# Optimization experiments

Measured on AMD Instinct MI355X. Metric: run time of the kernel, lower is better.

Reference implementation:

```python
import jax, jax.numpy as jnp
import numpy as np

NUM_EXPERTS = 16
TOP_K = 2
FFT_LEN = 512
SEQ_LEN = 512
PRED_LEN = 720
MOE_TEMP = 1.0


def setup_inputs() -> dict:
    key = jax.random.key(0)
    ks = jax.random.split(key, 5)
    x = jax.random.normal(ks[0], (8192, SEQ_LEN), dtype=jnp.float32)
    # gating network: Linear(fft_len//2 -> num_experts)
    gw = jax.random.normal(ks[1], (NUM_EXPERTS, FFT_LEN // 2), dtype=jnp.float32) * (1.0 / np.sqrt(FFT_LEN // 2))
    gb = jnp.zeros((NUM_EXPERTS,), dtype=jnp.float32)
    # experts: RLinear = instance-norm (RevIN) + Linear(seq->pred), stacked
    ew = jax.random.normal(ks[2], (NUM_EXPERTS, SEQ_LEN, PRED_LEN), dtype=jnp.float32) * (1.0 / np.sqrt(SEQ_LEN))
    eb = jnp.zeros((NUM_EXPERTS, PRED_LEN), dtype=jnp.float32)
    return {"x": x, "gw": gw, "gb": gb, "ew": ew, "eb": eb}


def periodogram(x, n):
    # x: [B, L] -> normalized power spectrum [B, n//2]
    x0 = x - jnp.mean(x, axis=1, keepdims=True)
    dft = jnp.fft.fft(x0, n=n, axis=1) / jnp.sqrt(jnp.asarray(n, x.dtype))
    I = jnp.abs(dft[:, : n // 2]) ** 2
    s = jnp.sum(I, axis=1, keepdims=True)
    s = jnp.where(s == 0, 1.0, s)
    return I / s


def expert_apply(x, ew, eb):
    # RLinear: instance normalize, linear map, de-normalize
    mu = jnp.mean(x, axis=1, keepdims=True)
    sd = jnp.std(x, axis=1, keepdims=True) + 1e-5
    xn = (x - mu) / sd  # [B, L]
    # all experts densely: [B,L] x [E,L,P] -> [E,B,P]
    y = jnp.einsum('bl,elp->ebp', xn, ew) + eb[:, None, :]
    return y * sd[None] + mu[None]  # [E, B, P]


def reference(x, gw, gb, ew, eb):
    I = periodogram(x, FFT_LEN)  # [B, n//2]
    gate = (I @ gw.T + gb) / MOE_TEMP  # eval mode: divide by temp, no noise
    topk_vals, topk_idx = jax.lax.top_k(gate, TOP_K)  # [B, k]
    gates = jax.nn.softmax(topk_vals, axis=1)  # [B, k]
    expert_out = expert_apply(x, ew, eb)  # [E, B, P]
    # gather selected experts: [B, k, P]
    sel = jnp.take_along_axis(
        jnp.transpose(expert_out, (1, 0, 2)), topk_idx[:, :, None], axis=1
    )
    return jnp.sum(gates[:, :, None] * sel, axis=1)  # [B, P]
```

## Files before the change

### kernel.cpp

```cpp
#include <hip/hip_runtime.h>
#include <hip/hip_bf16.h>
#include <math.h>

#define NEXP  16
#define SEQ   512
#define PRED  720
#define NROWS 8192
#define NFREQ 256

typedef __bf16 bf16x8 __attribute__((ext_vector_type(8)));
typedef float  f32x16 __attribute__((ext_vector_type(16)));

__device__ __forceinline__ void gload_lds16(const void* g, void* l) {
    __builtin_amdgcn_global_load_lds(
        (const __attribute__((address_space(1))) unsigned int*)g,
        (__attribute__((address_space(3))) unsigned int*)l, 16, 0, 0);
}

__device__ __forceinline__ int xcd_swizzle(int bid, int nwg) {
    const int q = nwg >> 3, r = nwg & 7;
    const int xcd = bid & 7, off = bid >> 3;
    return (xcd < r ? xcd * (q + 1) : r * (q + 1) + (xcd - r) * q) + off;
}

__global__ __launch_bounds__(256) void k_preproc(const float* __restrict__ ew,
                                                 const float* __restrict__ x,
                                                 __hip_bfloat16* __restrict__ ewt,
                                                 __hip_bfloat16* __restrict__ bthi,
                                                 __hip_bfloat16* __restrict__ btlo,
                                                 __hip_bfloat16* __restrict__ xn,
                                                 __hip_bfloat16* __restrict__ xnlo,
                                                 float* __restrict__ meta,
                                                 int* __restrict__ nredo)
{
    const int bid = blockIdx.x;
    const int t   = threadIdx.x;

    if (bid < 512) {
        if (bid == 0 && t == 0) *nredo = 0;
        const int tid  = bid * 256 + t;
        const int f    = tid >> 9;
        const int lidx = tid & 511;
        const int m    = (f * lidx) & 511;

        constexpr double Cj[9] = {0.9999247018391445033, 0.9996988186962042201,
                                  0.9987954562051723927, 0.9951847266721968862,
                                  0.9807852804032304491, 0.9238795325112867561,
                                  0.7071067811865475244, 0.0, -1.0};
        constexpr double Sj[9] = {0.0122715382857199261, 0.0245412285229122880,
                                  0.0490676743274180143, 0.0980171403295606020,
                                  0.1950903220161282678, 0.3826834323650897717,
                                  0.7071067811865475244, 1.0, 0.0};
        double cr = 1.0, ci = 0.0;
#pragma unroll
        for (int j = 0; j < 9; ++j) {
            const bool on = (m >> j) & 1;
            const double mr = on ? Cj[j] : 1.0;
            const double mi = on ? Sj[j] : 0.0;
            const double nr = cr * mr - ci * mi;
            ci = cr * mi + ci * mr;
            cr = nr;
        }
        const size_t c0 = (size_t)(2 * f) * 512 + lidx;
        const size_t c1 = (size_t)(2 * f + 1) * 512 + lidx;
        {
            __hip_bfloat16 h = __float2bfloat16((float)cr);
            float hif = __bfloat162float(h);
            bthi[c0] = h;
            btlo[c0] = __float2bfloat16((float)(cr - (double)hif));
        }
        {
            __hip_bfloat16 h = __float2bfloat16((float)ci);
            float hif = __bfloat162float(h);
            bthi[c1] = h;
            btlo[c1] = __float2bfloat16((float)(ci - (double)hif));
        }
        return;
    }

    if (bid < 6400) {
        __shared__ float tile[32][33];
        const int rel = bid - 512;
        const int e   = rel / 368;
        const int rem = rel % 368;
        const int p0  = (rem % 23) * 32;
        const int l0  = (rem / 23) * 32;
        const int tx  = t & 31;
        const int ty  = t >> 5;
        const float* src = ew + (size_t)e * SEQ * PRED;
#pragma unroll
        for (int i = 0; i < 4; ++i) {
            int l = l0 + ty + i * 8;
            int p = p0 + tx;
            tile[ty + i * 8][tx] = (p < PRED) ? src[(size_t)l * PRED + p] : 0.f;
        }
        __syncthreads();
        __hip_bfloat16* dst = ewt + (size_t)e * PRED * SEQ;
#pragma unroll
        for (int i = 0; i < 4; ++i) {
            int p = p0 + ty + i * 8;
            int l = l0 + tx;
            if (p < PRED) dst[(size_t)p * SEQ + l] = __float2bfloat16(tile[tx][ty + i * 8]);
        }
        return;
    }

    {
        const int wv = t >> 6, l = t & 63;
        const int b  = (bid - 6400) * 4 + wv;
        const float* xr = x + (size_t)b * SEQ;

        const float4 v0 = *(const float4*)(xr + l * 8);
        const float4 v1 = *(const float4*)(xr + l * 8 + 4);
        const double d0 = v0.x, d1 = v0.y, d2 = v0.z, d3 = v0.w;
        const double d4 = v1.x, d5 = v1.y, d6 = v1.z, d7 = v1.w;

        double s1 = ((d0 + d1) + (d2 + d3)) + ((d4 + d5) + (d6 + d7));
        double s2 = ((d0 * d0 + d1 * d1) + (d2 * d2 + d3 * d3)) +
                    ((d4 * d4 + d5 * d5) + (d6 * d6 + d7 * d7));
#pragma unroll
        for (int off = 1; off < 64; off <<= 1) {
            s1 += __shfl_xor(s1, off);
            s2 += __shfl_xor(s2, off);
        }
        const double mu = s1 * (1.0 / 512.0);
        double var = s2 * (1.0 / 512.0) - mu * mu;
        if (var < 0.0) var = 0.0;
        const double sd = sqrt(var) + 1e-5, inv = 1.0 / sd;

        unsigned int hw[4], lw[4];
#define CONV(j, dj)                                                         \
        {                                                                   \
            double xnd = (dj - mu) * inv;                                   \
            __hip_bfloat16 h = __float2bfloat16((float)xnd);                \
            float hif = __bfloat162float(h);                                \
            __hip_bfloat16 lo = __float2bfloat16((float)(xnd - (double)hif)); \
            unsigned int hb = *(unsigned short*)&h;                         \
            unsigned int lb = *(unsigned short*)&lo;                        \
            if ((j & 1) == 0) { hw[j >> 1] = hb; lw[j >> 1] = lb; }         \
            else { hw[j >> 1] |= hb << 16; lw[j >> 1] |= lb << 16; }        \
        }
        CONV(0, d0) CONV(1, d1) CONV(2, d2) CONV(3, d3)
        CONV(4, d4) CONV(5, d5) CONV(6, d6) CONV(7, d7)
#undef CONV
        *(uint4*)(xn   + (size_t)b * SEQ + l * 8) = uint4{hw[0], hw[1], hw[2], hw[3]};
        *(uint4*)(xnlo + (size_t)b * SEQ + l * 8) = uint4{lw[0], lw[1], lw[2], lw[3]};

        if (l == 0) {
            meta[b * 4 + 0] = (float)mu;
            meta[b * 4 + 3] = (float)sd;
        }
    }
}

__global__ __launch_bounds__(256, 3) void k_dft_gemm(
    const __hip_bfloat16* __restrict__ xn, const __hip_bfloat16* __restrict__ xnlo,
    const __hip_bfloat16* __restrict__ bthi, const __hip_bfloat16* __restrict__ btlo,
    float* __restrict__ Iout)
{
    const int wgid = xcd_swizzle(blockIdx.x, 512);
    const int rt = wgid >> 2;
    const int ct = wgid & 3;

    __shared__ __align__(16) __hip_bfloat16 As[2][64][64];
    __shared__ __align__(16) __hip_bfloat16 Bs[2][128][64];

    const int t  = threadIdx.x;
    const int wv = t >> 6, l = t & 63;

    size_t aoff[2], boff[4];
    int arow[2], achk[2], brow[4], bchk[4];
#pragma unroll
    for (int i = 0; i < 2; ++i) {
        const int idx = i * 256 + t;
        const int row = idx >> 3, chk = idx & 7;
        const int swz = (row & 7) ^ ((row & 8) >> 1);
        arow[i] = row; achk[i] = chk;
        aoff[i] = (size_t)(rt * 64 + row) * SEQ + (size_t)(chk ^ swz) * 8;
    }
#pragma unroll
    for (int i = 0; i < 4; ++i) {
        const int idx = i * 256 + t;
        const int row = idx >> 3, chk = idx & 7;
        const int swz = (row & 7) ^ ((row & 8) >> 1);
        brow[i] = row; bchk[i] = chk;
        boff[i] = (size_t)(ct * 128 + row) * SEQ + (size_t)(chk ^ swz) * 8;
    }

#define DSTAGE(buf, kk) do {                                                   \
    const int pass_ = (kk) >> 3;                                               \
    const int koff_ = ((kk) & 7) * 64;                                         \
    const __hip_bfloat16* ap_ = (pass_ == 1) ? xnlo : xn;                      \
    const __hip_bfloat16* bp_ = (pass_ == 2) ? btlo : bthi;                    \
    _Pragma("unroll")                                                          \
    for (int i_ = 0; i_ < 2; ++i_)                                             \
        gload_lds16(ap_ + aoff[i_] + koff_, &As[buf][arow[i_]][achk[i_] * 8]); \
    _Pragma("unroll")                                                          \
    for (int i_ = 0; i_ < 4; ++i_)                                             \
        gload_lds16(bp_ + boff[i_] + koff_, &Bs[buf][brow[i_]][bchk[i_] * 8]); \
} while (0)

    f32x16 acc[2];
#pragma unroll
    for (int ni = 0; ni < 2; ++ni)
#pragma unroll
        for (int q = 0; q < 16; ++q) acc[ni][q] = 0.f;

    const int wr = wv >> 1, wc = wv & 1;
    const int fl = l & 31, fh = l >> 5;
    const int rswz = (fl & 7) ^ ((fl & 8) >> 1);

    DSTAGE(0, 0);
    asm volatile("s_waitcnt vmcnt(0)" ::: "memory");
    __builtin_amdgcn_s_barrier();
#pragma unroll
    for (int kt = 0; kt < 24; ++kt) {
        const int cur = kt & 1;
        if (kt < 23) DSTAGE(cur ^ 1, kt + 1);
        __builtin_amdgcn_sched_barrier(0);
        __builtin_amdgcn_s_setprio(1);
#pragma unroll
        for (int ks = 0; ks < 4; ++ks) {
            const int cc = ((ks * 2 + fh) ^ rswz) * 8;
            const bf16x8 a  = *(const bf16x8*)&As[cur][wr * 32 + fl][cc];
            const bf16x8 b0 = *(const bf16x8*)&Bs[cur][wc * 64 + fl][cc];
            const bf16x8 b1 = *(const bf16x8*)&Bs[cur][wc * 64 + 32 + fl][cc];
            acc[0] = __builtin_amdgcn_mfma_f32_32x32x16_bf16(a, b0, acc[0], 0, 0, 0);
            acc[1] = __builtin_amdgcn_mfma_f32_32x32x16_bf16(a, b1, acc[1], 0, 0, 0);
        }
        __builtin_amdgcn_s_setprio(0);
        __builtin_amdgcn_sched_barrier(0);
        asm volatile("s_waitcnt vmcnt(0)" ::: "memory");
        __builtin_amdgcn_s_barrier();
    }
#undef DSTAGE

    const int crow_base = 4 * fh;
#pragma unroll
    for (int ni = 0; ni < 2; ++ni) {
        const int col = ct * 128 + wc * 64 + ni * 32 + fl;
#pragma unroll
        for (int q = 0; q < 16; ++q) {
            const float v = acc[ni][q];
            const float w = __shfl_xor(v, 1);
            if ((fl & 1) == 0) {
                const int rl = wr * 32 + (q & 3) + 8 * (q >> 2) + crow_base;
                Iout[(size_t)(rt * 64 + rl) * NFREQ + (col >> 1)] = v * v + w * w;
            }
        }
    }
}

__global__ __launch_bounds__(256) void k_gatefin(const float* __restrict__ Iout,
                                                 const float* __restrict__ gw,
                                                 const float* __restrict__ gb,
                                                 float* __restrict__ meta,
                                                 int* __restrict__ eidx,
                                                 int* __restrict__ redo,
                                                 int* __restrict__ nredo)
{
    __shared__ float gws[NEXP * 257];
    __shared__ float Pw[4][256];
    __shared__ float Gs[4][16];

    const int t  = threadIdx.x;
    const int wv = t >> 6, l = t & 63;
    const int b  = blockIdx.x * 4 + wv;

    for (int i = t; i < NEXP * NFREQ; i += 256)
        gws[(i >> 8) * 257 + (i & 255)] = gw[i];
    __syncthreads();

    const float* Ir = Iout + (size_t)b * NFREQ;
    const float i0 = Ir[l], i1 = Ir[64 + l], i2 = Ir[128 + l], i3 = Ir[192 + l];
    Pw[wv][l] = i0; Pw[wv][64 + l] = i1; Pw[wv][128 + l] = i2; Pw[wv][192 + l] = i3;
    float ps = (i0 + i1) + (i2 + i3);
#pragma unroll
    for (int off = 1; off < 64; off <<= 1) ps += __shfl_xor(ps, off);

    const int e = l >> 2, kb = l & 3;
    float acc = 0.f;
#pragma unroll 8
    for (int j = 0; j < 64; ++j) {
        const int k = kb + 4 * j;
        acc += Pw[wv][k] * gws[e * 257 + k];
    }
    acc += __shfl_xor(acc, 1);
    acc += __shfl_xor(acc, 2);
    if (kb == 0) Gs[wv][e] = acc;

    if (l == 0) {
        const float sdiv  = (ps == 0.f) ? 1.f : ps;
        const float inv_s = 1.f / sdiv;
        float b1 = -1e30f, b2 = -1e30f, b3 = -1e30f;
        int i1b = 0, i2b = 0;
#pragma unroll
        for (int i = 0; i < NEXP; ++i) {
            float v = Gs[wv][i] * inv_s + gb[i];
            if (v > b1)      { b3 = b2; b2 = b1; i2b = i1b; b1 = v; i1b = i; }
            else if (v > b2) { b3 = b2; b2 = v; i2b = i; }
            else if (v > b3) { b3 = v; }
        }
        if (b2 - b3 < 1e-4f * fmaxf(1.f, fabsf(b1))) {
            const int r = atomicAdd(nredo, 1);
            redo[r] = b;
        } else {
            const float sd = meta[b * 4 + 3];
            const float ee = __expf(b2 - b1);
            const float w0 = 1.f / (1.f + ee);
            const float w1 = ee / (1.f + ee);
            meta[b * 4 + 1] = w0 * sd;
            meta[b * 4 + 2] = w1 * sd;
            eidx[b * 2 + 0] = i1b;
            eidx[b * 2 + 1] = i2b;
        }
    }
}

__global__ __launch_bounds__(256, 4) void k_gate64(const float* __restrict__ x,
                                                   const float* __restrict__ gw,
                                                   const float* __restrict__ gb,
                                                   float* __restrict__ meta,
                                                   int* __restrict__ eidx,
                                                   const int* __restrict__ redo,
                                                   const int* __restrict__ nredo)
{
    __shared__ double Pw[4][256];
    __shared__ double Gs[4][16];

    const int t  = threadIdx.x;
    const int wv = t >> 6, l = t & 63;
    const int n  = *nredo;

    for (int it = blockIdx.x * 4 + wv; it < n; it += gridDim.x * 4) {
        const int b = redo[it];
        const float* xr = x + (size_t)b * SEQ;

        double s1 = 0.0, s2 = 0.0;
#define DLOADV(n_) double vr##n_ = (double)xr[64 * n_ + l]; s1 += vr##n_; s2 += vr##n_ * vr##n_;
        DLOADV(0) DLOADV(1) DLOADV(2) DLOADV(3) DLOADV(4) DLOADV(5) DLOADV(6) DLOADV(7)
#undef DLOADV
        double vi0, vi1, vi2, vi3, vi4, vi5, vi6, vi7;

#pragma unroll
        for (int off = 1; off < 64; off <<= 1) {
            s1 += __shfl_xor(s1, off);
            s2 += __shfl_xor(s2, off);
        }
        const double mu = s1 * (1.0 / 512.0);
        double var = s2 * (1.0 / 512.0) - mu * mu;
        if (var < 0.0) var = 0.0;
        const double sd = sqrt(var) + 1e-5;

#define DSUB(n_) vr##n_ -= mu;
        DSUB(0) DSUB(1) DSUB(2) DSUB(3) DSUB(4) DSUB(5) DSUB(6) DSUB(7)
#undef DSUB

        {
            const double C = 0.70710678118654752440084436210485;
            double a0 = vr0 + vr4, a1 = vr1 + vr5, a2 = vr2 + vr6, a3 = vr3 + vr7;
            double d0 = vr0 - vr4, d1 = vr1 - vr5, d2 = vr2 - vr6, d3 = vr3 - vr7;
            double c0 = a0 + a2, c2 = a0 - a2, c1 = a1 + a3;
            double c3i = a3 - a1;
            double e1r = C * (d1 - d3), e1i = -C * (d1 + d3);
            vr0 = c0 + c1;   vi0 = 0.0;
            vr1 = c0 - c1;   vi1 = 0.0;
            vr2 = c2;        vi2 = c3i;
            vr3 = c2;        vi3 = -c3i;
            vr4 = d0 + e1r;  vi4 = -d2 + e1i;
            vr5 = d0 - e1r;  vi5 = -d2 - e1i;
            vr6 = d0 - e1r;  vi6 =  d2 + e1i;
            vr7 = d0 + e1r;  vi7 =  d2 - e1i;
        }

        double w1r = 1.0, w1i = 0.0;
        {
            constexpr double Cr[6] = {0.9999247018391445033, 0.9996988186962042201,
                                      0.9987954562051723927, 0.9951847266721968862,
                                      0.9807852804032304491, 0.9238795325112867561};
            constexpr double Ci[6] = {-0.0122715382857199261, -0.0245412285229122880,
                                      -0.0490676743274180143, -0.0980171403295606020,
                                      -0.1950903220161282678, -0.3826834323650897717};
#pragma unroll
            for (int j = 0; j < 6; ++j) {
                const bool on = (l >> j) & 1;
                const double mr = on ? Cr[j] : 1.0;
                const double mi = on ? Ci[j] : 0.0;
                const double nr = w1r * mr - w1i * mi;
                w1i = w1r * mi + w1i * mr;
                w1r = nr;
            }
        }

        {
            double wkr = w1r, wki = w1i;
#define DTWID(n_) { double tr_ = vr##n_ * wkr - vi##n_ * wki; \
                    vi##n_ = vr##n_ * wki + vi##n_ * wkr; vr##n_ = tr_; }
#define DWSTEP() { double nr_ = wkr * w1r - wki * w1i; \
                   wki = wkr * w1i + wki * w1r; wkr = nr_; }
            DTWID(4) DWSTEP() DTWID(2) DWSTEP() DTWID(6) DWSTEP() DTWID(1)
            DWSTEP() DTWID(5) DWSTEP() DTWID(3) DWSTEP() DTWID(7)
#undef DTWID
#undef DWSTEP
        }

        double twr, twi;
        {
            double w2r = w1r * w1r - w1i * w1i, w2i = 2.0 * w1r * w1i;
            double w4r = w2r * w2r - w2i * w2i, w4i = 2.0 * w2r * w2i;
            twr = w4r * w4r - w4i * w4i; twi = 2.0 * w4r * w4i;
        }
#define DBF(R, I, h, hi, ter, tei) { \
        double br_ = __shfl_xor(R, h); double bi_ = __shfl_xor(I, h); \
        double dr_ = hi ? (R - br_) : (R + br_); \
        double di_ = hi ? (I - bi_) : (I + bi_); \
        R = dr_ * ter - di_ * tei; I = dr_ * tei + di_ * ter; }
#define DSTG(hc) { \
        const bool hi_ = (l & hc) != 0; \
        const double ter_ = hi_ ? twr : 1.0; \
        const double tei_ = hi_ ? twi : 0.0; \
        DBF(vr0, vi0, hc, hi_, ter_, tei_) DBF(vr1, vi1, hc, hi_, ter_, tei_) \
        DBF(vr2, vi2, hc, hi_, ter_, tei_) DBF(vr3, vi3, hc, hi_, ter_, tei_) \
        DBF(vr4, vi4, hc, hi_, ter_, tei_) DBF(vr5, vi5, hc, hi_, ter_, tei_) \
        DBF(vr6, vi6, hc, hi_, ter_, tei_) DBF(vr7, vi7, hc, hi_, ter_, tei_) \
        double ntr_ = twr * twr - twi * twi; twi = 2.0 * twr * twi; twr = ntr_; }
        DSTG(32) DSTG(16) DSTG(8) DSTG(4) DSTG(2) DSTG(1)
#undef DSTG
#undef DBF

        const int k2 = (int)(__brev((unsigned)l) >> 26);
        double ps = 0.0;
        if ((l & 1) == 0) {
            const int kb = 8 * k2;
            double P;
            P = vr0 * vr0 + vi0 * vi0; ps += P; Pw[wv][0 + kb] = P;
            P = vr1 * vr1 + vi1 * vi1; ps += P; Pw[wv][4 + kb] = P;
            P = vr2 * vr2 + vi2 * vi2; ps += P; Pw[wv][2 + kb] = P;
            P = vr3 * vr3 + vi3 * vi3; ps += P; Pw[wv][6 + kb] = P;
            P = vr4 * vr4 + vi4 * vi4; ps += P; Pw[wv][1 + kb] = P;
            P = vr5 * vr5 + vi5 * vi5; ps += P; Pw[wv][5 + kb] = P;
            P = vr6 * vr6 + vi6 * vi6; ps += P; Pw[wv][3 + kb] = P;
            P = vr7 * vr7 + vi7 * vi7; ps += P; Pw[wv][7 + kb] = P;
        }
#pragma unroll
        for (int off = 1; off < 64; off <<= 1) ps += __shfl_xor(ps, off);

        {
            const int e = l >> 2, kb = l & 3;
            double acc = 0.0;
#pragma unroll 8
            for (int j = 0; j < 64; ++j) {
                int k = kb + 4 * j;
                acc += Pw[wv][k] * (double)gw[e * NFREQ + k];
            }
            acc += __shfl_xor(acc, 1);
            acc += __shfl_xor(acc, 2);
            if (kb == 0) Gs[wv][e] = acc;
        }

        if (l == 0) {
            const double sdiv  = (ps == 0.0) ? 1.0 : ps;
            const double inv_s = 1.0 / sdiv;
            double best = -1e300, best2 = -1e300;
            int i0b = 0, i1b = 0;
#pragma unroll
            for (int i = 0; i < NEXP; ++i) {
                double v = Gs[wv][i] * inv_s + (double)gb[i];
                if (v > best)       { best2 = best; i1b = i0b; best = v; i0b = i; }
                else if (v > best2) { best2 = v; i1b = i; }
            }
            const double eexp = (double)__expf((float)(best2 - best));
            const double w0 = 1.0 / (1.0 + eexp);
            const double w1 = eexp / (1.0 + eexp);
            meta[b * 4 + 0] = (float)mu;
            meta[b * 4 + 1] = (float)(w0 * sd);
            meta[b * 4 + 2] = (float)(w1 * sd);
            meta[b * 4 + 3] = (float)sd;
            eidx[b * 2 + 0] = i0b;
            eidx[b * 2 + 1] = i1b;
        }
    }
}

__global__ __launch_bounds__(256) void k_count(const int* __restrict__ eidx,
                                               int* __restrict__ blockHist)
{
    __shared__ int h[32];
    const int t   = threadIdx.x;
    const int blk = blockIdx.x;
    if (t < 32) h[t] = 0;
    __syncthreads();
    const int b  = blk * 256 + t;
    const int e0 = eidx[2 * b];
    const int e1 = eidx[2 * b + 1];
    atomicAdd(&h[e0], 1);
    atomicAdd(&h[16 + e1], 1);
    __syncthreads();
    if (t < 32) blockHist[(t >> 4) * 512 + blk * 16 + (t & 15)] = h[t];
}

__global__ void k_scan(const int* __restrict__ blockHist, int* __restrict__ counts,
                       int* __restrict__ offs, int* __restrict__ tdesc,
                       int* __restrict__ base)
{
    __shared__ int cnt[32];
    __shared__ int off_s[32];
    const int j = threadIdx.x;
    if (j < 32) {
        const int s = j >> 4, e = j & 15;
        int acc = 0;
        for (int blk = 0; blk < 32; ++blk) acc += blockHist[s * 512 + blk * 16 + e];
        cnt[j] = acc;
        counts[j] = acc;
    }
    __syncthreads();
    if (j < 2) {
        int acc = 0, tt = 0;
        for (int i = 0; i < NEXP; ++i) {
            const int c = cnt[j * 16 + i];
            off_s[j * 16 + i] = acc;
            offs[j * 16 + i]  = acc;
            acc += c;
            const int nt = (c + 63) >> 6;
            for (int k = 0; k < nt; ++k) tdesc[j * 160 + tt++] = (i << 16) | k;
        }
        for (; tt < 160; ++tt) tdesc[j * 160 + tt] = -1;
    }
    __syncthreads();
    if (j < 32) {
        const int s = j >> 4, e = j & 15;
        int run = off_s[j];
        for (int blk = 0; blk < 32; ++blk) {
            base[s * 512 + blk * 16 + e] = run;
            run += blockHist[s * 512 + blk * 16 + e];
        }
    }
}

__global__ __launch_bounds__(256) void k_scatter(const int* __restrict__ eidx,
                                                 const int* __restrict__ base,
                                                 int* __restrict__ lists)
{
    __shared__ int whist[2][4][16];
    const int t   = threadIdx.x;
    const int wv  = t >> 6, l = t & 63;
    const int blk = blockIdx.x;
    const int b   = blk * 256 + t;
    const int e0  = eidx[2 * b];
    const int e1  = eidx[2 * b + 1];
    const unsigned long long before = (1ULL << l) - 1ULL;

    unsigned long long m0 = 0, m1 = 0;
#pragma unroll
    for (int bb = 0; bb < 16; ++bb) {
        unsigned long long m = __ballot(e0 == bb);
        if (e0 == bb) m0 = m;
        if (l == 0) whist[0][wv][bb] = __popcll(m);
    }
#pragma unroll
    for (int bb = 0; bb < 16; ++bb) {
        unsigned long long m = __ballot(e1 == bb);
        if (e1 == bb) m1 = m;
        if (l == 0) whist[1][wv][bb] = __popcll(m);
    }
    __syncthreads();

    int p0 = __popcll(m0 & before);
    int p1 = __popcll(m1 & before);
    for (int w = 0; w < 4; ++w) {
        if (w < wv) {
            p0 += whist[0][w][e0];
            p1 += whist[1][w][e1];
        }
    }
    lists[base[blk * 16 + e0] + p0]                 = b;
    lists[NROWS + base[512 + blk * 16 + e1] + p1]   = b;
}

__global__ __launch_bounds__(256, 3) void k_expert_gemm(
    const __hip_bfloat16* __restrict__ xn, const __hip_bfloat16* __restrict__ ewt,
    const float* __restrict__ eb, const float* __restrict__ meta,
    const int* __restrict__ lists, const int* __restrict__ offs,
    const int* __restrict__ counts, const int* __restrict__ tdesc,
    float* __restrict__ out, float* __restrict__ out2)
{
    const int wgid = xcd_swizzle(blockIdx.x, 1920);
    const int slot = wgid / 960;
    const int rem  = wgid - slot * 960;
    const int tid  = rem / 6;
    const int ct   = rem % 6;
    const int d    = tdesc[slot * 160 + tid];
    if (d < 0) return;
    const int e  = d >> 16;
    const int rt = d & 0xffff;
    const int n_e = counts[slot * NEXP + e];

    __shared__ __align__(16) __hip_bfloat16 As[2][64][64];
    __shared__ __align__(16) __hip_bfloat16 Bs[2][128][64];
    __shared__ int   rowB[64];
    __shared__ float rowMu[64];
    __shared__ float rowC[64];

    const int t  = threadIdx.x;
    const int wv = t >> 6, l = t & 63;
    const int* list = lists + slot * NROWS + offs[slot * NEXP + e];
    if (t < 64) {
        int r  = rt * 64 + t;
        int bb = (r < n_e) ? list[r] : -1;
        rowB[t]  = bb;
        rowMu[t] = (bb >= 0) ? meta[bb * 4] : 0.f;
        rowC[t]  = (bb >= 0) ? meta[bb * 4 + 1 + slot] : 0.f;
    }
    __syncthreads();

    const __hip_bfloat16* asrc[2];
    const __hip_bfloat16* bsrc[4];
    int arow[2], achk[2], brow[4], bchk[4];
#pragma unroll
    for (int i = 0; i < 2; ++i) {
        const int idx = i * 256 + t;
        const int row = idx >> 3, chk = idx & 7;
        const int swz = (row & 7) ^ ((row & 8) >> 1);
        arow[i] = row; achk[i] = chk;
        const int ab = rowB[row];
        asrc[i] = xn + ((ab >= 0) ? (size_t)ab * SEQ : 0) + (size_t)(chk ^ swz) * 8;
    }
#pragma unroll
    for (int i = 0; i < 4; ++i) {
        const int idx = i * 256 + t;
        const int row = idx >> 3, chk = idx & 7;
        const int swz = (row & 7) ^ ((row & 8) >> 1);
        brow[i] = row; bchk[i] = chk;
        const int gc  = ct * 128 + row;
        const int gcc = (gc < PRED) ? gc : (PRED - 1);
        bsrc[i] = ewt + ((size_t)e * PRED + gcc) * SEQ + (size_t)(chk ^ swz) * 8;
    }

#define STAGE(buf, koff) do {                                                  \
    _Pragma("unroll")                                                          \
    for (int i_ = 0; i_ < 2; ++i_)                                             \
        gload_lds16(asrc[i_] + (koff), &As[buf][arow[i_]][achk[i_] * 8]);      \
    _Pragma("unroll")                                                          \
    for (int i_ = 0; i_ < 4; ++i_)                                             \
        gload_lds16(bsrc[i_] + (koff), &Bs[buf][brow[i_]][bchk[i_] * 8]);      \
} while (0)

    f32x16 acc[2];
#pragma unroll
    for (int ni = 0; ni < 2; ++ni)
#pragma unroll
        for (int q = 0; q < 16; ++q) acc[ni][q] = 0.f;

    const int wr = wv >> 1, wc = wv & 1;
    const int fl = l & 31, fh = l >> 5;
    const int rswz = (fl & 7) ^ ((fl & 8) >> 1);

    STAGE(0, 0);
    asm volatile("s_waitcnt vmcnt(0)" ::: "memory");
    __builtin_amdgcn_s_barrier();
#pragma unroll
    for (int kt = 0; kt < 8; ++kt) {
        const int cur = kt & 1;
        if (kt < 7) STAGE(cur ^ 1, (kt + 1) * 64);
        __builtin_amdgcn_sched_barrier(0);
        __builtin_amdgcn_s_setprio(1);
#pragma unroll
        for (int ks = 0; ks < 4; ++ks) {
            const int cc = ((ks * 2 + fh) ^ rswz) * 8;
            const bf16x8 a  = *(const bf16x8*)&As[cur][wr * 32 + fl][cc];
            const bf16x8 b0 = *(const bf16x8*)&Bs[cur][wc * 64 + fl][cc];
            const bf16x8 b1 = *(const bf16x8*)&Bs[cur][wc * 64 + 32 + fl][cc];
            acc[0] = __builtin_amdgcn_mfma_f32_32x32x16_bf16(a, b0, acc[0], 0, 0, 0);
            acc[1] = __builtin_amdgcn_mfma_f32_32x32x16_bf16(a, b1, acc[1], 0, 0, 0);
        }
        __builtin_amdgcn_s_setprio(0);
        __builtin_amdgcn_sched_barrier(0);
        asm volatile("s_waitcnt vmcnt(0)" ::: "memory");
        __builtin_amdgcn_s_barrier();
    }
#undef STAGE

    const int crow_base = 4 * fh;
#pragma unroll
    for (int ni = 0; ni < 2; ++ni) {
        const int col = ct * 128 + wc * 64 + ni * 32 + fl;
        const bool cok = (col < PRED);
        const float ebv = cok ? eb[e * PRED + col] : 0.f;
#pragma unroll
        for (int q = 0; q < 16; ++q) {
            const int rl = wr * 32 + (q & 3) + 8 * (q >> 2) + crow_base;
            const int bb = rowB[rl];
            if (!cok || bb < 0) continue;
            const float v = acc[ni][q] + ebv;
            if (slot == 0) out [(size_t)bb * PRED + col] = rowMu[rl] + rowC[rl] * v;
            else           out2[(size_t)bb * PRED + col] = rowC[rl] * v;
        }
    }
}

__global__ __launch_bounds__(256) void k_merge(float* __restrict__ out,
                                               const float* __restrict__ out2)
{
    const int i = blockIdx.x * 256 + threadIdx.x;
    float4 a = ((float4*)out)[i];
    const float4 b = ((const float4*)out2)[i];
    a.x += b.x; a.y += b.y; a.z += b.z; a.w += b.w;
    ((float4*)out)[i] = a;
}

extern "C" void kernel_launch(void* const* d_in, const int* in_sizes, int n_in,
                              void* d_out, int out_size, void* d_ws, size_t ws_size,
                              hipStream_t stream)
{
    const float* x  = (const float*)d_in[0];
    const float* gw = (const float*)d_in[1];
    const float* gb = (const float*)d_in[2];
    const float* ew = (const float*)d_in[3];
    const float* eb = (const float*)d_in[4];
    float* out = (float*)d_out;
    char*  ws  = (char*)d_ws;

    constexpr size_t XN_OFF   = 0;
    constexpr size_t XN_SZ    = (size_t)NROWS * SEQ * 2;
    constexpr size_t XNLO_OFF = XN_OFF + XN_SZ;
    constexpr size_t EWT_OFF  = XNLO_OFF + XN_SZ;
    constexpr size_t EWT_SZ   = (size_t)NEXP * PRED * SEQ * 2;
    constexpr size_t BTHI_OFF = EWT_OFF + EWT_SZ;
    constexpr size_t BT_SZ    = (size_t)512 * 512 * 2;
    constexpr size_t BTLO_OFF = BTHI_OFF + BT_SZ;
    constexpr size_t IOUT_OFF = BTLO_OFF + BT_SZ;
    constexpr size_t IOUT_SZ  = (size_t)NROWS * NFREQ * 4;
    constexpr size_t META_OFF = IOUT_OFF + IOUT_SZ;
    constexpr size_t META_SZ  = (size_t)NROWS * 4 * 4;
    constexpr size_t EIDX_OFF = META_OFF + META_SZ;
    constexpr size_t EIDX_SZ  = (size_t)NROWS * 2 * 4;
    constexpr size_t LIST_OFF = EIDX_OFF + EIDX_SZ;
    constexpr size_t LIST_SZ  = (size_t)2 * NROWS * 4;
    constexpr size_t CNT_OFF  = LIST_OFF + LIST_SZ;
    constexpr size_t OFFS_OFF = CNT_OFF + 144;
    constexpr size_t TDSC_OFF = OFFS_OFF + 128;
    constexpr size_t BH_OFF   = TDSC_OFF + 1280;
    constexpr size_t BASE_OFF = BH_OFF + 4096;
    constexpr size_t REDO_OFF = BASE_OFF + 4096;
    constexpr size_t OUT2_OFF = REDO_OFF + (size_t)NROWS * 4;

    __hip_bfloat16* xn   = (__hip_bfloat16*)(ws + XN_OFF);
    __hip_bfloat16* xnlo = (__hip_bfloat16*)(ws + XNLO_OFF);
    __hip_bfloat16* ewt  = (__hip_bfloat16*)(ws + EWT_OFF);
    __hip_bfloat16* bthi = (__hip_bfloat16*)(ws + BTHI_OFF);
    __hip_bfloat16* btlo = (__hip_bfloat16*)(ws + BTLO_OFF);
    float* Iout  = (float*)(ws + IOUT_OFF);
    float* meta  = (float*)(ws + META_OFF);
    int* eidx    = (int*)(ws + EIDX_OFF);
    int* lists   = (int*)(ws + LIST_OFF);
    int* counts  = (int*)(ws + CNT_OFF);
    int* nredo   = (int*)(ws + CNT_OFF + 128);
    int* offs    = (int*)(ws + OFFS_OFF);
    int* tdesc   = (int*)(ws + TDSC_OFF);
    int* bhist   = (int*)(ws + BH_OFF);
    int* base    = (int*)(ws + BASE_OFF);
    int* redo    = (int*)(ws + REDO_OFF);
    float* out2  = (float*)(ws + OUT2_OFF);

    k_preproc<<<dim3(8448), dim3(256), 0, stream>>>(ew, x, ewt, bthi, btlo,
                                                    xn, xnlo, meta, nredo);
    k_dft_gemm<<<dim3(512), dim3(256), 0, stream>>>(xn, xnlo, bthi, btlo, Iout);
    k_gatefin<<<dim3(NROWS / 4), dim3(256), 0, stream>>>(Iout, gw, gb, meta, eidx,
                                                         redo, nredo);
    k_gate64<<<dim3(64), dim3(256), 0, stream>>>(x, gw, gb, meta, eidx, redo, nredo);
    k_count<<<dim3(32), dim3(256), 0, stream>>>(eidx, bhist);
    k_scan<<<dim3(1), dim3(64), 0, stream>>>(bhist, counts, offs, tdesc, base);
    k_scatter<<<dim3(32), dim3(256), 0, stream>>>(eidx, base, lists);
    k_expert_gemm<<<dim3(1920), dim3(256), 0, stream>>>(
        xn, ewt, eb, meta, lists, offs, counts, tdesc, out, out2);
    k_merge<<<dim3(NROWS * PRED / 1024), dim3(256), 0, stream>>>(out, out2);
}
```

Baseline: 141.4 us.

## Replace out2 buffer and merge kernel with atomic accumulation into zeroed output

Extra blocks in the preprocessing kernel now zero the output, and the expert GEMM atomically adds both top-k contributions straight into it. This drops the second output buffer and the separate merge kernel, which read and wrote the full output again. The gating-finish kernel also handles 16 rows per block instead of 4, so the gate weight matrix is staged into LDS fewer times. The cost is scattered float atomics in the GEMM epilogue and a summation order that depends on which slot finishes first.

Measured after the change: 164.0 us. 16.0% more time.

```diff
diff --git a/kernel.cpp b/kernel.cpp
--- a/kernel.cpp
+++ b/kernel.cpp
@@ -31,7 +31,8 @@
                                                  __hip_bfloat16* __restrict__ xn,
                                                  __hip_bfloat16* __restrict__ xnlo,
                                                  float* __restrict__ meta,
-                                                 int* __restrict__ nredo)
+                                                 int* __restrict__ nredo,
+                                                 float* __restrict__ out)
 {
     const int bid = blockIdx.x;
     const int t   = threadIdx.x;
@@ -105,7 +106,7 @@
         return;
     }
 
-    {
+    if (bid < 8448) {
         const int wv = t >> 6, l = t & 63;
         const int b  = (bid - 6400) * 4 + wv;
         const float* xr = x + (size_t)b * SEQ;
@@ -150,6 +151,15 @@
             meta[b * 4 + 0] = (float)mu;
             meta[b * 4 + 3] = (float)sd;
         }
+        return;
+    }
+
+    {
+        const size_t base = ((size_t)(bid - 8448) * 256 + t) * 16;
+        float4 z = {0.f, 0.f, 0.f, 0.f};
+#pragma unroll
+        for (int i = 0; i < 4; ++i)
+            *(float4*)(out + base + i * 4) = z;
     }
 }
 
@@ -265,54 +275,56 @@
 
     const int t  = threadIdx.x;
     const int wv = t >> 6, l = t & 63;
-    const int b  = blockIdx.x * 4 + wv;
 
     for (int i = t; i < NEXP * NFREQ; i += 256)
         gws[(i >> 8) * 257 + (i & 255)] = gw[i];
     __syncthreads();
 
-    const float* Ir = Iout + (size_t)b * NFREQ;
-    const float i0 = Ir[l], i1 = Ir[64 + l], i2 = Ir[128 + l], i3 = Ir[192 + l];
-    Pw[wv][l] = i0; Pw[wv][64 + l] = i1; Pw[wv][128 + l] = i2; Pw[wv][192 + l] = i3;
-    float ps = (i0 + i1) + (i2 + i3);
-#pragma unroll
-    for (int off = 1; off < 64; off <<= 1) ps += __shfl_xor(ps, off);
-
-    const int e = l >> 2, kb = l & 3;
-    float acc = 0.f;
+    for (int r = 0; r < 4; ++r) {
+        const int b = blockIdx.x * 16 + wv * 4 + r;
+        const float* Ir = Iout + (size_t)b * NFREQ;
+        const float i0 = Ir[l], i1 = Ir[64 + l], i2 = Ir[128 + l], i3 = Ir[192 + l];
+        Pw[wv][l] = i0; Pw[wv][64 + l] = i1; Pw[wv][128 + l] = i2; Pw[wv][192 + l] = i3;
+        float ps = (i0 + i1) + (i2 + i3);
+#pragma unroll
+        for (int off = 1; off < 64; off <<= 1) ps += __shfl_xor(ps, off);
+
+        const int e = l >> 2, kb = l & 3;
+        float acc = 0.f;
 #pragma unroll 8
-    for (int j = 0; j < 64; ++j) {
-        const int k = kb + 4 * j;
-        acc += Pw[wv][k] * gws[e * 257 + k];
-    }
-    acc += __shfl_xor(acc, 1);
-    acc += __shfl_xor(acc, 2);
-    if (kb == 0) Gs[wv][e] = acc;
-
-    if (l == 0) {
-        const float sdiv  = (ps == 0.f) ? 1.f : ps;
-        const float inv_s = 1.f / sdiv;
-        float b1 = -1e30f, b2 = -1e30f, b3 = -1e30f;
-        int i1b = 0, i2b = 0;
-#pragma unroll
-        for (int i = 0; i < NEXP; ++i) {
-            float v = Gs[wv][i] * inv_s + gb[i];
-            if (v > b1)      { b3 = b2; b2 = b1; i2b = i1b; b1 = v; i1b = i; }
-            else if (v > b2) { b3 = b2; b2 = v; i2b = i; }
-            else if (v > b3) { b3 = v; }
-        }
-        if (b2 - b3 < 1e-4f * fmaxf(1.f, fabsf(b1))) {
-            const int r = atomicAdd(nredo, 1);
-            redo[r] = b;
-        } else {
-            const float sd = meta[b * 4 + 3];
-            const float ee = __expf(b2 - b1);
-            const float w0 = 1.f / (1.f + ee);
-            const float w1 = ee / (1.f + ee);
-            meta[b * 4 + 1] = w0 * sd;
-            meta[b * 4 + 2] = w1 * sd;
-            eidx[b * 2 + 0] = i1b;
-            eidx[b * 2 + 1] = i2b;
+        for (int j = 0; j < 64; ++j) {
+            const int k = kb + 4 * j;
+            acc += Pw[wv][k] * gws[e * 257 + k];
+        }
+        acc += __shfl_xor(acc, 1);
+        acc += __shfl_xor(acc, 2);
+        if (kb == 0) Gs[wv][e] = acc;
+
+        if (l == 0) {
+            const float sdiv  = (ps == 0.f) ? 1.f : ps;
+            const float inv_s = 1.f / sdiv;
+            float b1 = -1e30f, b2 = -1e30f, b3 = -1e30f;
+            int i1b = 0, i2b = 0;
+#pragma unroll
+            for (int i = 0; i < NEXP; ++i) {
+                float v = Gs[wv][i] * inv_s + gb[i];
+                if (v > b1)      { b3 = b2; b2 = b1; i2b = i1b; b1 = v; i1b = i; }
+                else if (v > b2) { b3 = b2; b2 = v; i2b = i; }
+                else if (v > b3) { b3 = v; }
+            }
+            if (b2 - b3 < 1e-4f * fmaxf(1.f, fabsf(b1))) {
+                const int rr = atomicAdd(nredo, 1);
+                redo[rr] = b;
+            } else {
+                const float sd = meta[b * 4 + 3];
+                const float ee = __expf(b2 - b1);
+                const float w0 = 1.f / (1.f + ee);
+                const float w1 = ee / (1.f + ee);
+                meta[b * 4 + 1] = w0 * sd;
+                meta[b * 4 + 2] = w1 * sd;
+                eidx[b * 2 + 0] = i1b;
+                eidx[b * 2 + 1] = i2b;
+            }
         }
     }
 }
@@ -582,7 +594,7 @@
     const float* __restrict__ eb, const float* __restrict__ meta,
     const int* __restrict__ lists, const int* __restrict__ offs,
     const int* __restrict__ counts, const int* __restrict__ tdesc,
-    float* __restrict__ out, float* __restrict__ out2)
+    float* __restrict__ out)
 {
     const int wgid = xcd_swizzle(blockIdx.x, 1920);
     const int slot = wgid / 960;
@@ -692,20 +704,11 @@
             const int bb = rowB[rl];
             if (!cok || bb < 0) continue;
             const float v = acc[ni][q] + ebv;
-            if (slot == 0) out [(size_t)bb * PRED + col] = rowMu[rl] + rowC[rl] * v;
-            else           out2[(size_t)bb * PRED + col] = rowC[rl] * v;
-        }
-    }
-}
-
-__global__ __launch_bounds__(256) void k_merge(float* __restrict__ out,
-                                               const float* __restrict__ out2)
-{
-    const int i = blockIdx.x * 256 + threadIdx.x;
-    float4 a = ((float4*)out)[i];
-    const float4 b = ((const float4*)out2)[i];
-    a.x += b.x; a.y += b.y; a.z += b.z; a.w += b.w;
-    ((float4*)out)[i] = a;
+            const float contrib = (slot == 0) ? (rowMu[rl] + rowC[rl] * v)
+                                              : (rowC[rl] * v);
+            atomicAdd(out + (size_t)bb * PRED + col, contrib);
+        }
+    }
 }
 
 extern "C" void kernel_launch(void* const* d_in, const int* in_sizes, int n_in,
@@ -742,7 +745,6 @@
     constexpr size_t BH_OFF   = TDSC_OFF + 1280;
     constexpr size_t BASE_OFF = BH_OFF + 4096;
     constexpr size_t REDO_OFF = BASE_OFF + 4096;
-    constexpr size_t OUT2_OFF = REDO_OFF + (size_t)NROWS * 4;
 
     __hip_bfloat16* xn   = (__hip_bfloat16*)(ws + XN_OFF);
     __hip_bfloat16* xnlo = (__hip_bfloat16*)(ws + XNLO_OFF);
@@ -760,18 +762,16 @@
     int* bhist   = (int*)(ws + BH_OFF);
     int* base    = (int*)(ws + BASE_OFF);
     int* redo    = (int*)(ws + REDO_OFF);
-    float* out2  = (float*)(ws + OUT2_OFF);
-
-    k_preproc<<<dim3(8448), dim3(256), 0, stream>>>(ew, x, ewt, bthi, btlo,
-                                                    xn, xnlo, meta, nredo);
+
+    k_preproc<<<dim3(9888), dim3(256), 0, stream>>>(ew, x, ewt, bthi, btlo,
+                                                    xn, xnlo, meta, nredo, out);
     k_dft_gemm<<<dim3(512), dim3(256), 0, stream>>>(xn, xnlo, bthi, btlo, Iout);
-    k_gatefin<<<dim3(NROWS / 4), dim3(256), 0, stream>>>(Iout, gw, gb, meta, eidx,
-                                                         redo, nredo);
+    k_gatefin<<<dim3(NROWS / 16), dim3(256), 0, stream>>>(Iout, gw, gb, meta, eidx,
+                                                          redo, nredo);
     k_gate64<<<dim3(64), dim3(256), 0, stream>>>(x, gw, gb, meta, eidx, redo, nredo);
     k_count<<<dim3(32), dim3(256), 0, stream>>>(eidx, bhist);
     k_scan<<<dim3(1), dim3(64), 0, stream>>>(bhist, counts, offs, tdesc, base);
     k_scatter<<<dim3(32), dim3(256), 0, stream>>>(eidx, base, lists);
     k_expert_gemm<<<dim3(1920), dim3(256), 0, stream>>>(
-        xn, ewt, eb, meta, lists, offs, counts, tdesc, out, out2);
-    k_merge<<<dim3(NROWS * PRED / 1024), dim3(256), 0, stream>>>(out, out2);
-}
+        xn, ewt, eb, meta, lists, offs, counts, tdesc, out);
+}
```
